# Performance work log

Measured on AMD Instinct MI355X. Metric: run time of the kernel, lower is better.

Reference implementation:

```python
import jax, jax.numpy as jnp
import numpy as np

A_NUM = 9
C_NUM = 20


def generate_anchor(anc, grid):
    # anc: (A,2) w,h ; grid: (B,H,W,2) centers -> anchors (B,A,H,W,4)
    centers = grid[:, None]                      # (B,1,H,W,2)
    half = anc.reshape(1, -1, 1, 1, 2) * 0.5     # (1,A,1,1,2)
    return jnp.concatenate([centers - half, centers + half], axis=-1)


def iou_matrix(proposals, bboxes):
    # proposals: (B,A,H,W,4) -> (B,K,4); bboxes: (B,N,5)
    B = proposals.shape[0]
    p = proposals.reshape(B, -1, 4)[:, :, None, :]   # (B,K,1,4)
    bb = bboxes[:, None, :, :]                       # (B,1,N,5)
    s_p = (p[..., 2] - p[..., 0]) * (p[..., 3] - p[..., 1])
    s_b = (bb[..., 2] - bb[..., 0]) * (bb[..., 3] - bb[..., 1])
    ix1 = jnp.maximum(p[..., 0], bb[..., 0])
    iy1 = jnp.maximum(p[..., 1], bb[..., 1])
    ix2 = jnp.minimum(p[..., 2], bb[..., 2])
    iy2 = jnp.minimum(p[..., 3], bb[..., 3])
    s_i = jnp.clip(ix2 - ix1, 0.0) * jnp.clip(iy2 - iy1, 0.0)
    s_u = s_p + s_b - s_i
    iou = jnp.clip(s_i / (s_u + 1e-8), 0.0)
    invalid = (s_u <= 0) | (s_p <= 0) | (s_b <= 0) | (bb[..., 0] < 0)
    return jnp.where(invalid, 0.0, iou)              # (B,K,N)


def extract_anchor_data(anchor_data, idx):
    # anchor_data: (B,A,D,H,W) -> flat (B*A*H*W, D) -> gather
    B, A, D, H, W = anchor_data.shape
    flat = jnp.transpose(anchor_data, (0, 1, 3, 4, 2)).reshape(-1, D)
    return flat[idx]


def extract_class_scores(all_scores, idx, num_anchors):
    # all_scores: (B,C,H,W) -> (B,A,H,W,C) flat -> gather
    B, C, H, W = all_scores.shape
    s = jnp.transpose(all_scores, (0, 2, 3, 1))[:, None]          # (B,1,H,W,C)
    s = jnp.broadcast_to(s, (B, num_anchors, H, W, C)).reshape(-1, C)
    return s[idx]


def setup_inputs() -> dict:
    key = jax.random.key(0)
    ks = jax.random.split(key, 8)
    B, Cin, H, W = 32, 1280, 28, 28
    N, M = 64, 4096
    hid, out_ch = 128, 5 * A_NUM + C_NUM
    features = jax.random.normal(ks[0], (B, Cin, H, W), dtype=jnp.float32)
    # grid of feature-cell centers (GenerateGrid-style)
    xs = jnp.arange(W, dtype=jnp.float32) + 0.5
    ys = jnp.arange(H, dtype=jnp.float32) + 0.5
    gx, gy = jnp.meshgrid(xs, ys, indexing='xy')
    grid = jnp.broadcast_to(jnp.stack([gx, gy], axis=-1), (B, H, W, 2))
    anc = jnp.array([[1.0, 1], [2, 2], [3, 3], [4, 4], [5, 5], [2, 3], [3, 2], [3, 5], [5, 3]], dtype=jnp.float32)
    tl = jax.random.uniform(ks[1], (B, N, 2), minval=0.0, maxval=20.0)
    wh = jax.random.uniform(ks[2], (B, N, 2), minval=1.0, maxval=8.0)
    cls = jax.random.randint(ks[3], (B, N, 1), 0, C_NUM).astype(jnp.float32)
    bb = jnp.concatenate([tl, tl + wh, cls], axis=-1)
    valid = jax.random.uniform(ks[4], (B, N, 1)) > 0.25
    bboxes = jnp.where(valid, bb, -1.0)
    K = B * A_NUM * H * W
    pos_anchor_idx = jax.random.randint(ks[5], (M,), 0, K, dtype=jnp.int64 if jax.config.jax_enable_x64 else jnp.int32)
    neg_anchor_idx = jax.random.randint(ks[6], (M,), 0, K, dtype=pos_anchor_idx.dtype)
    W1 = jax.random.normal(ks[7], (hid, Cin), dtype=jnp.float32) * 0.02
    b1 = jnp.zeros((hid,), dtype=jnp.float32)
    W2 = jax.random.normal(jax.random.fold_in(key, 99), (out_ch, hid), dtype=jnp.float32) * 0.02
    b2 = jnp.zeros((out_ch,), dtype=jnp.float32)
    return {"features": features, "grid": grid, "anc": anc, "bboxes": bboxes,
            "pos_anchor_idx": pos_anchor_idx, "neg_anchor_idx": neg_anchor_idx,
            "W1": W1, "b1": b1, "W2": W2, "b2": b2}


def reference(features, grid, anc, bboxes, pos_anchor_idx, neg_anchor_idx, W1, b1, W2, b2):
    B, Cin, H, W = features.shape
    A, C = A_NUM, C_NUM
    # anchors + broadcast IoU matrix
    anchors = generate_anchor(anc, grid)                 # (B,A,H,W,4)
    iou_mat = iou_matrix(anchors, bboxes)                # (B,A*H*W,N)
    # prediction head: 1x1 conv -> (dropout eval: identity) -> leaky_relu -> 1x1 conv
    h = jnp.einsum('bchw,oc->bohw', features, W1) + b1[None, :, None, None]
    h = jax.nn.leaky_relu(h, negative_slope=0.01)
    out = jnp.einsum('bchw,oc->bohw', h, W2) + b2[None, :, None, None]  # (B,5A+C,H,W)
    anchor_raw = out[:, :5 * A].reshape(B, A, 5, H, W)
    conf_sq = jax.nn.sigmoid(anchor_raw[:, :, 0:1])      # (B,A,1,H,W)
    off_raw = anchor_raw[:, :, 1:]                       # (B,A,4,H,W)
    off_sq = jnp.concatenate([jax.nn.sigmoid(off_raw[:, :, :2]) - 0.5, off_raw[:, :, 2:]], axis=2)
    class_raw = out[:, 5 * A:]                           # (B,C,H,W)
    # training path: irregular gathers
    class_scores = extract_class_scores(class_raw, pos_anchor_idx, A)   # (M,C)
    offsets = extract_anchor_data(off_sq, pos_anchor_idx)               # (M,4)
    conf_pos = extract_anchor_data(conf_sq, pos_anchor_idx)             # (M,1)
    conf_neg = extract_anchor_data(conf_sq, neg_anchor_idx)             # (M,1)
    conf_scores = jnp.concatenate([conf_pos, conf_neg], axis=0)         # (2M,1)
    return conf_scores, offsets, class_scores, iou_mat
```

## Files before the change

### kernel.cpp

```cpp
#include <hip/hip_runtime.h>
#include <cstdint>

#define A_NUM 9
#define C_NUM 20
#define B_SZ 32
#define HW 784
#define P_NUM (A_NUM*HW)
#define NBOX 64
#define CIN 1280
#define HID 128
#define M_IDX 4096
#define KS_ALL 40
#define ASTR3 36
#define HSTR2 136
#define OSTR 80
#define IOU_PB 64

#define CONF_OFF 0
#define OFFS_OFF (2*M_IDX)
#define CLS_OFF  (OFFS_OFF + 4*M_IDX)
#define IOU_OFF  (CLS_OFF + C_NUM*M_IDX)

#define GEMM_MT 25
#define GEMM_BLKS (GEMM_MT*B_SZ)
#define IOU_BX ((P_NUM + IOU_PB - 1)/IOU_PB)
#define IOU_BLKS (IOU_BX*B_SZ)

typedef short bf16x8 __attribute__((ext_vector_type(8)));
typedef float f32x4  __attribute__((ext_vector_type(4)));

__device__ __forceinline__ unsigned pack_bf16(float lo, float hi) {
  unsigned a = __builtin_bit_cast(unsigned, lo);
  unsigned b = __builtin_bit_cast(unsigned, hi);
  return ((a + 0x8000u) >> 16) | ((b + 0x8000u) & 0xffff0000u);
}

__global__ __launch_bounds__(256) void prep_w(const float* __restrict__ W1,
                                              const float* __restrict__ W2,
                                              uint4* __restrict__ W1f,
                                              uint4* __restrict__ W2f) {
  int id = blockIdx.x * 256 + threadIdx.x;
  if (id < 20480) {
    int lane = id & 63;
    int ntile = (id >> 6) & 7;
    int ks = id >> 9;
    int lo = lane & 15, quad = lane >> 4;
    int n = ntile * 16 + lo;
    int k0 = ks * 32 + quad * 8;
    const float* src = W1 + n * CIN + k0;
    float4 x = *(const float4*)src;
    float4 y = *(const float4*)(src + 4);
    uint4 p;
    p.x = pack_bf16(x.x, x.y);
    p.y = pack_bf16(x.z, x.w);
    p.z = pack_bf16(y.x, y.y);
    p.w = pack_bf16(y.z, y.w);
    W1f[id] = p;
  } else {
    int i2 = id - 20480;
    int lane = i2 & 63;
    int ntile = (i2 >> 6) % 5;
    int ks = i2 / 320;
    int lo = lane & 15, quad = lane >> 4;
    int n = ntile * 16 + lo;
    int k0 = ks * 32 + quad * 8;
    uint4 p = (uint4){0, 0, 0, 0};
    if (n < 5 * A_NUM + C_NUM) {
      const float* src = W2 + n * HID + k0;
      float4 x = *(const float4*)src;
      float4 y = *(const float4*)(src + 4);
      p.x = pack_bf16(x.x, x.y);
      p.y = pack_bf16(x.z, x.w);
      p.z = pack_bf16(y.x, y.y);
      p.w = pack_bf16(y.z, y.w);
    }
    W2f[i2] = p;
  }
}

union SharedU {
  struct {
    float As[2][32 * ASTR3];
    unsigned short h[32 * HSTR2];
  } g;
  struct { float sb[NBOX * 5]; float4 sp4[IOU_PB]; } i;
};

__global__ __launch_bounds__(256) void fused_main(
    const float* __restrict__ F, const uint4* __restrict__ W1f,
    const uint4* __restrict__ W2f, const float* __restrict__ b1,
    const float* __restrict__ b2, float* __restrict__ Hd,
    const float* __restrict__ gridc, const float* __restrict__ anc,
    const float* __restrict__ bboxes, float* __restrict__ iou_out) {
  __shared__ SharedU sh;
  const int bid = blockIdx.x;
  const int t = threadIdx.x;

  if (bid >= GEMM_BLKS) {
    const int bid2 = bid - GEMM_BLKS;
    const int b = bid2 / IOU_BX;
    const int p0 = (bid2 - b * IOU_BX) * IOU_PB;
    float* sb = sh.i.sb;
    float4* sp4 = sh.i.sp4;
    for (int i = t; i < NBOX * 5; i += 256) sb[i] = bboxes[b * NBOX * 5 + i];
    if (t < IOU_PB) {
      int p = p0 + t;
      float x1 = 0.f, y1 = 0.f, x2 = 0.f, y2 = 0.f;
      if (p < P_NUM) {
        int a = p / HW, hw = p - a * HW;
        float2 c = ((const float2*)gridc)[b * HW + hw];
        float hx = anc[a * 2 + 0] * 0.5f, hy = anc[a * 2 + 1] * 0.5f;
        x1 = c.x - hx; y1 = c.y - hy; x2 = c.x + hx; y2 = c.y + hy;
      }
      sp4[t] = make_float4(x1, y1, x2, y2);
    }
    __syncthreads();
    const int nl = (t & 15) * 4;
    const int pi = t >> 4;
#pragma unroll
    for (int ip = 0; ip < 4; ip++) {
      const int pl = pi + 16 * ip;
      const int p = p0 + pl;
      const float4 pb = sp4[pl];
      const float spA = (pb.z - pb.x) * (pb.w - pb.y);
      float4 res;
#pragma unroll
      for (int jn = 0; jn < 4; jn++) {
        const int n = nl + jn;
        float bx1 = sb[n * 5 + 0], by1 = sb[n * 5 + 1];
        float bx2 = sb[n * 5 + 2], by2 = sb[n * 5 + 3];
        float s_b = (bx2 - bx1) * (by2 - by1);
        float ix1 = fmaxf(pb.x, bx1), iy1 = fmaxf(pb.y, by1);
        float ix2 = fminf(pb.z, bx2), iy2 = fminf(pb.w, by2);
        float si = fmaxf(ix2 - ix1, 0.f) * fmaxf(iy2 - iy1, 0.f);
        float su = spA + s_b - si;
        float iou = fmaxf(si / (su + 1e-8f), 0.f);
        bool invalid = (su <= 0.f) | (spA <= 0.f) | (s_b <= 0.f) | (bx1 < 0.f);
        float v = invalid ? 0.f : iou;
        if (jn == 0) res.x = v; else if (jn == 1) res.y = v;
        else if (jn == 2) res.z = v; else res.w = v;
      }
      if (p < P_NUM)
        *(float4*)&iou_out[((size_t)(b * P_NUM + p)) * 64 + nl] = res;
    }
    return;
  }

  const int w = t >> 6, lane = t & 63;
  const int quad = lane >> 4, lo = lane & 15;
  const int b = bid / GEMM_MT;
  const int mt = bid - b * GEMM_MT;
  const int m0 = mt * 32;

  const int cl = t >> 3;
  const int mq = t & 7;
  const int mld = min(m0 + 4 * mq, HW - 4);
  const float* Fb = F + ((size_t)b * CIN + cl) * HW + mld;

  f32x4 acc[2][2];
#pragma unroll
  for (int i = 0; i < 2; i++)
#pragma unroll
    for (int j = 0; j < 2; j++) acc[i][j] = (f32x4){0.f, 0.f, 0.f, 0.f};

  float4 rg[3];
  uint4 vb[3][2];

  auto loadF = [&](int kk, float4* r) {
    *r = *(const float4*)(Fb + (size_t)kk * 32 * HW);
  };
  auto loadB = [&](int kk, uint4* v) {
    const uint4* p = W1f + (size_t)kk * 512 + 2 * w * 64 + lane;
    v[0] = p[0];
    v[1] = p[64];
  };
  auto stage = [&](int buf, const float4& r) {
    float* d = &sh.g.As[buf][(4 * mq) * ASTR3 + cl];
    d[0] = r.x; d[ASTR3] = r.y; d[2 * ASTR3] = r.z; d[3 * ASTR3] = r.w;
  };
  auto compute = [&](int buf, uint4* v) {
    const float* Ab = &sh.g.As[buf][lo * ASTR3 + quad * 8];
#pragma unroll
    for (int i = 0; i < 2; i++) {
      f32x4 a0 = *(const f32x4*)(Ab + i * 16 * ASTR3);
      f32x4 a1 = *(const f32x4*)(Ab + i * 16 * ASTR3 + 4);
      uint4 ap;
      ap.x = pack_bf16(a0[0], a0[1]);
      ap.y = pack_bf16(a0[2], a0[3]);
      ap.z = pack_bf16(a1[0], a1[1]);
      ap.w = pack_bf16(a1[2], a1[3]);
      bf16x8 af = __builtin_bit_cast(bf16x8, ap);
#pragma unroll
      for (int nf = 0; nf < 2; nf++)
        acc[i][nf] = __builtin_amdgcn_mfma_f32_16x16x32_bf16(
            af, __builtin_bit_cast(bf16x8, v[nf]), acc[i][nf], 0, 0, 0);
    }
  };

  loadF(0, &rg[0]); loadF(1, &rg[1]);
  loadB(0, vb[0]); loadB(1, vb[1]);
  stage(0, rg[0]);
  __syncthreads();
#pragma unroll
  for (int kk = 0; kk < KS_ALL; kk++) {
    const int cur = kk & 1;
    if (kk + 2 < KS_ALL) {
      loadF(kk + 2, &rg[(kk + 2) % 3]);
      loadB(kk + 2, vb[(kk + 2) % 3]);
    }
    compute(cur, vb[kk % 3]);
    if (kk + 1 < KS_ALL) stage(cur ^ 1, rg[(kk + 1) % 3]);
    __syncthreads();
  }

#pragma unroll
  for (int i = 0; i < 2; i++) {
#pragma unroll
    for (int nf = 0; nf < 2; nf++) {
      const int n = w * 32 + nf * 16 + lo;
      const float bb = b1[n];
#pragma unroll
      for (int r = 0; r < 4; r++) {
        float v = acc[i][nf][r] + bb;
        v = v > 0.f ? v : 0.01f * v;
        unsigned u = __builtin_bit_cast(unsigned, v);
        sh.g.h[(i * 16 + quad * 4 + r) * HSTR2 + n] =
            (unsigned short)((u + 0x8000u) >> 16);
      }
    }
  }
  __syncthreads();

  for (int id = w; id < 10; id += 4) {
    const int mf = id / 5, nt = id - (id / 5) * 5;
    f32x4 acc2 = (f32x4){0.f, 0.f, 0.f, 0.f};
#pragma unroll
    for (int k2 = 0; k2 < 4; k2++) {
      bf16x8 haf = *(const bf16x8*)&sh.g.h[(mf * 16 + lo) * HSTR2 + k2 * 32 + quad * 8];
      bf16x8 bf = __builtin_bit_cast(bf16x8, W2f[(k2 * 5 + nt) * 64 + lane]);
      acc2 = __builtin_amdgcn_mfma_f32_16x16x32_bf16(haf, bf, acc2, 0, 0, 0);
    }
    const int o = nt * 16 + lo;
    if (o < 5 * A_NUM + C_NUM) {
      const float bz = b2[o];
      const int t5 = (o < 5 * A_NUM) ? (o % 5) : 5;
      const int mrow = m0 + mf * 16 + quad * 4;
#pragma unroll
      for (int r = 0; r < 4; r++) {
        const int m = mrow + r;
        if (m < HW) {
          float v = acc2[r] + bz;
          if (t5 == 0) v = 1.f / (1.f + expf(-v));
          else if (t5 == 1 || t5 == 2) v = 1.f / (1.f + expf(-v)) - 0.5f;
          Hd[((size_t)b * HW + m) * OSTR + o] = v;
        }
      }
    }
  }
}

__global__ __launch_bounds__(256) void gather2(
    const int* __restrict__ pos_idx, const int* __restrict__ neg_idx,
    const float* __restrict__ Hd, float* __restrict__ out) {
  const int bid = blockIdx.x;
  if (bid < M_IDX / 8) {
    const int g = threadIdx.x >> 5;
    const int l = threadIdx.x & 31;
    const int slot = bid * 8 + g;
    const int idx = pos_idx[slot];
    const int b = idx / P_NUM, r = idx - b * P_NUM;
    const int a = r / HW, hw = r - a * HW;
    const float* row = Hd + ((size_t)b * HW + hw) * OSTR;
    if (l == 0)       out[CONF_OFF + slot] = row[a * 5];
    else if (l < 5)   out[OFFS_OFF + slot * 4 + (l - 1)] = row[a * 5 + l];
    else if (l < 25)  out[CLS_OFF + slot * C_NUM + (l - 5)] = row[5 * A_NUM + (l - 5)];
  } else {
    const int tt = (bid - M_IDX / 8) * 256 + threadIdx.x;
    if (tt < M_IDX) {
      const int idx = neg_idx[tt];
      const int b = idx / P_NUM, r = idx - b * P_NUM;
      const int a = r / HW, hw = r - a * HW;
      out[CONF_OFF + M_IDX + tt] = Hd[((size_t)b * HW + hw) * OSTR + a * 5];
    }
  }
}

extern "C" void kernel_launch(void* const* d_in, const int* in_sizes, int n_in,
                              void* d_out, int out_size, void* d_ws, size_t ws_size,
                              hipStream_t stream) {
  const float* features = (const float*)d_in[0];
  const float* gridc    = (const float*)d_in[1];
  const float* anc      = (const float*)d_in[2];
  const float* bboxes   = (const float*)d_in[3];
  const int*   pos_idx  = (const int*)d_in[4];
  const int*   neg_idx  = (const int*)d_in[5];
  const float* W1       = (const float*)d_in[6];
  const float* b1       = (const float*)d_in[7];
  const float* W2       = (const float*)d_in[8];
  const float* b2       = (const float*)d_in[9];
  float* out = (float*)d_out;

  uint4* W1f = (uint4*)d_ws;
  uint4* W2f = (uint4*)((char*)d_ws + 327680);
  float* Hd  = (float*)((char*)d_ws + 327680 + 20480);

  hipLaunchKernelGGL(prep_w, dim3(85), dim3(256), 0, stream, W1, W2, W1f, W2f);
  hipLaunchKernelGGL(fused_main, dim3(GEMM_BLKS + IOU_BLKS), dim3(256), 0, stream,
                     features, W1f, W2f, b1, b2, Hd,
                     gridc, anc, bboxes, out + IOU_OFF);
  hipLaunchKernelGGL(gather2, dim3(M_IDX / 8 + 16), dim3(256), 0, stream,
                     pos_idx, neg_idx, Hd, out);
}
```

Measured before the change: 243.4 us.

## Stage bf16-packed A tiles in swizzled LDS with 128-wide K steps

Restructures the first GEMM's main loop. Each step now covers 128 input channels instead of 32, cutting the step count from 40 to 10 and with it the number of barriers. Activations are converted to bf16 once when written to LDS rather than on every read, and the LDS layout is XOR-swizzled so 128-bit fragment loads avoid bank conflicts. The barrier waits only on lgkmcnt rather than a full __syncthreads. In exchange, more registers are held for prefetch (8 B fragments plus 8 A vectors), which may reduce occupancy, and the W1 fragments are loaded in the same step they are consumed, exposing their latency.

```diff
diff --git a/kernel.cpp b/kernel.cpp
--- a/kernel.cpp
+++ b/kernel.cpp
@@ -10,8 +10,7 @@
 #define CIN 1280
 #define HID 128
 #define M_IDX 4096
-#define KS_ALL 40
-#define ASTR3 36
+#define NSTEP 10
 #define HSTR2 136
 #define OSTR 80
 #define IOU_PB 64
@@ -28,11 +27,19 @@
 
 typedef short bf16x8 __attribute__((ext_vector_type(8)));
 typedef float f32x4  __attribute__((ext_vector_type(4)));
+typedef unsigned u32x2 __attribute__((ext_vector_type(2)));
 
 __device__ __forceinline__ unsigned pack_bf16(float lo, float hi) {
   unsigned a = __builtin_bit_cast(unsigned, lo);
   unsigned b = __builtin_bit_cast(unsigned, hi);
   return ((a + 0x8000u) >> 16) | ((b + 0x8000u) & 0xffff0000u);
+}
+
+__device__ __forceinline__ void lds_barrier() {
+  asm volatile("s_waitcnt lgkmcnt(0)" ::: "memory");
+  __builtin_amdgcn_sched_barrier(0);
+  __builtin_amdgcn_s_barrier();
+  __builtin_amdgcn_sched_barrier(0);
 }
 
 __global__ __launch_bounds__(256) void prep_w(const float* __restrict__ W1,
@@ -80,7 +87,7 @@
 
 union SharedU {
   struct {
-    float As[2][32 * ASTR3];
+    unsigned Ab[2][32 * 64];
     unsigned short h[32 * HSTR2];
   } g;
   struct { float sb[NBOX * 5]; float4 sp4[IOU_PB]; } i;
@@ -152,10 +159,10 @@
   const int mt = bid - b * GEMM_MT;
   const int m0 = mt * 32;
 
-  const int cl = t >> 3;
-  const int mq = t & 7;
-  const int mld = min(m0 + 4 * mq, HW - 4);
-  const float* Fb = F + ((size_t)b * CIN + cl) * HW + mld;
+  const int m4 = t & 7;
+  const int kq = t >> 3;
+  const int mld = min(m0 + 4 * m4, HW - 4);
+  const float* Fb = F + ((size_t)b * CIN + 4 * kq) * HW + mld;
 
   f32x4 acc[2][2];
 #pragma unroll
@@ -163,54 +170,66 @@
 #pragma unroll
     for (int j = 0; j < 2; j++) acc[i][j] = (f32x4){0.f, 0.f, 0.f, 0.f};
 
-  float4 rg[3];
-  uint4 vb[3][2];
-
-  auto loadF = [&](int kk, float4* r) {
-    *r = *(const float4*)(Fb + (size_t)kk * 32 * HW);
+  f32x4 ra0[4], ra1[4];
+  uint4 vb[8];
+
+  auto loadA = [&](int s, f32x4* ra) {
+    const float* p = Fb + (size_t)s * 128 * HW;
+    ra[0] = *(const f32x4*)p;
+    ra[1] = *(const f32x4*)(p + HW);
+    ra[2] = *(const f32x4*)(p + 2 * HW);
+    ra[3] = *(const f32x4*)(p + 3 * HW);
   };
-  auto loadB = [&](int kk, uint4* v) {
-    const uint4* p = W1f + (size_t)kk * 512 + 2 * w * 64 + lane;
-    v[0] = p[0];
-    v[1] = p[64];
+  auto loadB = [&](int s) {
+    const uint4* p = W1f + (size_t)(4 * s) * 512 + 2 * w * 64 + lane;
+#pragma unroll
+    for (int j = 0; j < 4; j++) {
+      vb[2 * j]     = p[(size_t)j * 512];
+      vb[2 * j + 1] = p[(size_t)j * 512 + 64];
+    }
   };
-  auto stage = [&](int buf, const float4& r) {
-    float* d = &sh.g.As[buf][(4 * mq) * ASTR3 + cl];
-    d[0] = r.x; d[ASTR3] = r.y; d[2 * ASTR3] = r.z; d[3 * ASTR3] = r.w;
+  auto stage = [&](unsigned* buf, const f32x4* ra) {
+#pragma unroll
+    for (int r = 0; r < 4; r++) {
+      const int m = 4 * m4 + r;
+      unsigned d0 = pack_bf16(ra[0][r], ra[1][r]);
+      unsigned d1 = pack_bf16(ra[2][r], ra[3][r]);
+      const int off = m * 64 + (((kq >> 1) ^ (m & 15)) << 2) + 2 * (kq & 1);
+      *(u32x2*)(buf + off) = (u32x2){d0, d1};
+    }
   };
-  auto compute = [&](int buf, uint4* v) {
-    const float* Ab = &sh.g.As[buf][lo * ASTR3 + quad * 8];
-#pragma unroll
-    for (int i = 0; i < 2; i++) {
-      f32x4 a0 = *(const f32x4*)(Ab + i * 16 * ASTR3);
-      f32x4 a1 = *(const f32x4*)(Ab + i * 16 * ASTR3 + 4);
-      uint4 ap;
-      ap.x = pack_bf16(a0[0], a0[1]);
-      ap.y = pack_bf16(a0[2], a0[3]);
-      ap.z = pack_bf16(a1[0], a1[1]);
-      ap.w = pack_bf16(a1[2], a1[3]);
-      bf16x8 af = __builtin_bit_cast(bf16x8, ap);
-#pragma unroll
-      for (int nf = 0; nf < 2; nf++)
-        acc[i][nf] = __builtin_amdgcn_mfma_f32_16x16x32_bf16(
-            af, __builtin_bit_cast(bf16x8, v[nf]), acc[i][nf], 0, 0, 0);
+  auto compute = [&](const unsigned* buf) {
+#pragma unroll
+    for (int j = 0; j < 4; j++) {
+      const int u0 = ((j * 4 + quad) ^ lo) << 2;
+      bf16x8 a0 = *(const bf16x8*)(buf + lo * 64 + u0);
+      bf16x8 a1 = *(const bf16x8*)(buf + (lo + 16) * 64 + u0);
+      acc[0][0] = __builtin_amdgcn_mfma_f32_16x16x32_bf16(
+          a0, __builtin_bit_cast(bf16x8, vb[2 * j]), acc[0][0], 0, 0, 0);
+      acc[0][1] = __builtin_amdgcn_mfma_f32_16x16x32_bf16(
+          a0, __builtin_bit_cast(bf16x8, vb[2 * j + 1]), acc[0][1], 0, 0, 0);
+      acc[1][0] = __builtin_amdgcn_mfma_f32_16x16x32_bf16(
+          a1, __builtin_bit_cast(bf16x8, vb[2 * j]), acc[1][0], 0, 0, 0);
+      acc[1][1] = __builtin_amdgcn_mfma_f32_16x16x32_bf16(
+          a1, __builtin_bit_cast(bf16x8, vb[2 * j + 1]), acc[1][1], 0, 0, 0);
     }
   };
 
-  loadF(0, &rg[0]); loadF(1, &rg[1]);
-  loadB(0, vb[0]); loadB(1, vb[1]);
-  stage(0, rg[0]);
-  __syncthreads();
-#pragma unroll
-  for (int kk = 0; kk < KS_ALL; kk++) {
-    const int cur = kk & 1;
-    if (kk + 2 < KS_ALL) {
-      loadF(kk + 2, &rg[(kk + 2) % 3]);
-      loadB(kk + 2, vb[(kk + 2) % 3]);
-    }
-    compute(cur, vb[kk % 3]);
-    if (kk + 1 < KS_ALL) stage(cur ^ 1, rg[(kk + 1) % 3]);
-    __syncthreads();
+  loadA(0, ra0);
+  loadA(1, ra1);
+  stage(sh.g.Ab[0], ra0);
+  lds_barrier();
+#pragma unroll
+  for (int s = 0; s < NSTEP; s++) {
+    f32x4* raN = (s & 1) ? ra1 : ra0;
+    f32x4* raS = (s & 1) ? ra0 : ra1;
+    unsigned* bufC = sh.g.Ab[s & 1];
+    unsigned* bufN = sh.g.Ab[(s & 1) ^ 1];
+    if (s + 2 < NSTEP) loadA(s + 2, raN);
+    loadB(s);
+    if (s + 1 < NSTEP) stage(bufN, raS);
+    compute(bufC);
+    lds_barrier();
   }
 
 #pragma unroll
```

After: 243.0 us. Within noise of the previous version (-0.2%).
